# Kernel tuning notes

Measured on AMD Instinct MI355X. Metric: run time of the kernel, lower is better.

Reference implementation:

```python
import jax, jax.numpy as jnp
import numpy as np

TIME_STEPS = 100
MIN_LATENCY = 0
MAX_LATENCY = 99
THRESHOLD = 0.5
NOISE_STD = 0.01


def setup_inputs() -> dict:
    key = jax.random.key(0)
    k1, k2 = jax.random.split(key)
    x = jax.random.normal(k1, (256, 4096), dtype=jnp.float32)
    noise = jax.random.normal(k2, (256, 4096), dtype=jnp.float32)
    return {"x": x, "noise": noise}


def reference(x, noise):
    # x, noise: [B, F]
    x_noisy = x + noise * NOISE_STD
    x_norm = jax.nn.sigmoid(x_noisy)
    latencies = MIN_LATENCY + (1.0 - x_norm) * (MAX_LATENCY - MIN_LATENCY)
    latencies = jnp.clip(jnp.round(latencies).astype(jnp.int32), MIN_LATENCY, MAX_LATENCY)
    should_spike = x_norm > THRESHOLD                      # [B, F] bool
    # vectorized one-hot scatter: spikes[b, f, latencies[b, f]] = 1 if should_spike
    one_hot = jax.nn.one_hot(latencies, TIME_STEPS, dtype=jnp.float32)  # [B, F, T]
    spikes = one_hot * should_spike[..., None].astype(jnp.float32)
    return spikes
```

## Files before the change

### kernel.cpp

```cpp
#include <hip/hip_runtime.h>


#define T 100
#define PAIRS_PER_WAVE 64
#define PAIRS_PER_BLOCK 256
#define F4_PER_LANE 25

__global__ __launch_bounds__(256) void latency_encode_kernel(
    const float* __restrict__ x, const float* __restrict__ noise,
    float* __restrict__ out, int npairs) {
  const int tid  = threadIdx.x;
  const int lane = tid & 63;
  const int wave = tid >> 6;
  const long long waveBase =
      (long long)blockIdx.x * PAIRS_PER_BLOCK + (long long)wave * PAIRS_PER_WAVE;
  const long long p = waveBase + lane;

  int lat = -1;
  if (p < npairs) {
    double xn = (double)x[p] + (double)noise[p] * 0.01;
    double s  = 1.0 / (1.0 + exp(-xn));
    int li = (int)rint((1.0 - s) * 99.0);
    li = li < 0 ? 0 : (li > 99 ? 99 : li);
    lat = (s > 0.5) ? li : -1;
  }

  float4* o4 = (float4*)(out + waveBase * T);
  const float4 z = make_float4(0.f, 0.f, 0.f, 0.f);
  if (waveBase + PAIRS_PER_WAVE <= npairs) {
#pragma unroll
    for (int k = 0; k < F4_PER_LANE; ++k) o4[lane + k * 64] = z;
  } else if (waveBase < npairs) {
    const long long lim4 = ((long long)npairs - waveBase) * T / 4;
#pragma unroll
    for (int k = 0; k < F4_PER_LANE; ++k) {
      const int fi4 = lane + k * 64;
      if (fi4 < lim4) o4[fi4] = z;
    }
  }

  asm volatile("s_waitcnt vmcnt(0)" ::: "memory");

  if (lat >= 0) out[p * T + lat] = 1.0f;
}

extern "C" void kernel_launch(void* const* d_in, const int* in_sizes, int n_in,
                              void* d_out, int out_size, void* d_ws, size_t ws_size,
                              hipStream_t stream) {
  const float* x = (const float*)d_in[0];
  const float* noise = (const float*)d_in[1];
  float* out = (float*)d_out;
  const int npairs = in_sizes[0];
  const int grid = (npairs + PAIRS_PER_BLOCK - 1) / PAIRS_PER_BLOCK;
  latency_encode_kernel<<<grid, 256, 0, stream>>>(x, noise, out, npairs);
}
```

Baseline: 95.12 us.

## Split fused zero-fill and spike scatter into two grid-stride kernels

Replaces the single fused kernel, where each wave zeroed its own output slab and then scattered spikes, with two launches. The first is a grid-stride float4 zero-fill of the whole output and the second is a grid-stride kernel that computes latencies and writes the ones. This removes the per-wave vmcnt wait and the branchy tail handling, and lets the zero-fill run as a plain streaming write. In exchange it adds a second kernel launch, and the scatter writes then hit memory after the fill has finished rather than staying cache-local.

```diff
diff --git a/kernel.cpp b/kernel.cpp
--- a/kernel.cpp
+++ b/kernel.cpp
@@ -2,46 +2,26 @@
 
 
 #define T 100
-#define PAIRS_PER_WAVE 64
-#define PAIRS_PER_BLOCK 256
-#define F4_PER_LANE 25
 
-__global__ __launch_bounds__(256) void latency_encode_kernel(
+__global__ __launch_bounds__(256) void zero_fill_kernel(float4* __restrict__ o4, int n4) {
+  const int stride = gridDim.x * 256;
+  const float4 z = make_float4(0.f, 0.f, 0.f, 0.f);
+  for (int i = blockIdx.x * 256 + threadIdx.x; i < n4; i += stride) o4[i] = z;
+}
+
+__global__ __launch_bounds__(256) void spike_scatter_kernel(
     const float* __restrict__ x, const float* __restrict__ noise,
     float* __restrict__ out, int npairs) {
-  const int tid  = threadIdx.x;
-  const int lane = tid & 63;
-  const int wave = tid >> 6;
-  const long long waveBase =
-      (long long)blockIdx.x * PAIRS_PER_BLOCK + (long long)wave * PAIRS_PER_WAVE;
-  const long long p = waveBase + lane;
-
-  int lat = -1;
-  if (p < npairs) {
+  const int stride = gridDim.x * 256;
+  for (int p = blockIdx.x * 256 + threadIdx.x; p < npairs; p += stride) {
     double xn = (double)x[p] + (double)noise[p] * 0.01;
     double s  = 1.0 / (1.0 + exp(-xn));
-    int li = (int)rint((1.0 - s) * 99.0);
-    li = li < 0 ? 0 : (li > 99 ? 99 : li);
-    lat = (s > 0.5) ? li : -1;
-  }
-
-  float4* o4 = (float4*)(out + waveBase * T);
-  const float4 z = make_float4(0.f, 0.f, 0.f, 0.f);
-  if (waveBase + PAIRS_PER_WAVE <= npairs) {
-#pragma unroll
-    for (int k = 0; k < F4_PER_LANE; ++k) o4[lane + k * 64] = z;
-  } else if (waveBase < npairs) {
-    const long long lim4 = ((long long)npairs - waveBase) * T / 4;
-#pragma unroll
-    for (int k = 0; k < F4_PER_LANE; ++k) {
-      const int fi4 = lane + k * 64;
-      if (fi4 < lim4) o4[fi4] = z;
+    if (s > 0.5) {
+      int li = (int)rint((1.0 - s) * 99.0);
+      li = li < 0 ? 0 : (li > 99 ? 99 : li);
+      out[(long long)p * T + li] = 1.0f;
     }
   }
-
-  asm volatile("s_waitcnt vmcnt(0)" ::: "memory");
-
-  if (lat >= 0) out[p * T + lat] = 1.0f;
 }
 
 extern "C" void kernel_launch(void* const* d_in, const int* in_sizes, int n_in,
@@ -51,6 +31,8 @@
   const float* noise = (const float*)d_in[1];
   float* out = (float*)d_out;
   const int npairs = in_sizes[0];
-  const int grid = (npairs + PAIRS_PER_BLOCK - 1) / PAIRS_PER_BLOCK;
-  latency_encode_kernel<<<grid, 256, 0, stream>>>(x, noise, out, npairs);
+  const int n4 = out_size / 4;
+
+  zero_fill_kernel<<<2048, 256, 0, stream>>>((float4*)out, n4);
+  spike_scatter_kernel<<<1024, 256, 0, stream>>>(x, noise, out, npairs);
 }
```

Result: slower. 133.5 us (+40.3%).
